# Kernel tuning notes

Hardware: AMD Instinct MI355X
Metric: run time of the kernel (lower is better)

Reference implementation:

```python
import jax, jax.numpy as jnp
import numpy as np

K = 8  # 2^3 kernel offsets for kernel-size-2, stride-2 transposed conv in 3D (HYPER_CUBE)
HID = 64


def sp_convT(x, W, parent, kofs):
    """Sparse generative transposed conv via kernel map.
    x: [Nin, Cin]; W: [K, Cin, Cout]; parent: [Nout] int; kofs: [Nout] int in [0,K).
    out[j] = x[parent[j]] @ W[kofs[j]].
    """
    xg = x[parent]  # [Nout, Cin] gather
    out = jnp.zeros((parent.shape[0], W.shape[2]), dtype=x.dtype)
    for k in range(K):  # fixed small structural loop over kernel offsets
        out = out + jnp.where((kofs == k)[:, None], xg @ W[k], jnp.zeros((), x.dtype))
    return out


def setup_inputs() -> dict:
    key = jax.random.key(0)
    ks = jax.random.split(key, 12)
    Ns = [5000, 20000, 80000, 320000]
    sc_i = 1.0 / np.sqrt(64)
    inp = {
        'x0': jax.random.normal(ks[0], (Ns[0], 64), jnp.float32),
        'x1': jax.random.normal(ks[1], (Ns[1], 64), jnp.float32),
        'x2': jax.random.normal(ks[2], (Ns[2], 64), jnp.float32),
        'W_i': jax.random.normal(ks[3], (K, 64, 4 * HID), jnp.float32) * sc_i,
        'W_h': jax.random.normal(ks[4], (K, HID, 4 * HID), jnp.float32) * sc_i,
        'W_c': jax.random.normal(ks[5], (K, HID, HID), jnp.float32) * sc_i,
        'parent0': jax.random.randint(ks[6], (Ns[1],), 0, Ns[0], jnp.int32),
        'kofs0': jax.random.randint(ks[7], (Ns[1],), 0, K, jnp.int32),
        'parent1': jax.random.randint(ks[8], (Ns[2],), 0, Ns[1], jnp.int32),
        'kofs1': jax.random.randint(ks[9], (Ns[2],), 0, K, jnp.int32),
        'parent2': jax.random.randint(ks[10], (Ns[3],), 0, Ns[2], jnp.int32),
        'kofs2': jax.random.randint(ks[11], (Ns[3],), 0, K, jnp.int32),
    }
    return inp


def reference(x0, x1, x2, W_i, W_h, W_c, parent0, kofs0, parent1, kofs1, parent2, kofs2):
    xs = [x0, x1, x2]
    parents = [parent0, parent1, parent2]
    kofss = [kofs0, kofs1, kofs2]
    hx = jnp.zeros((x0.shape[0], HID), dtype=x0.dtype)
    cx = jnp.zeros((x0.shape[0], HID), dtype=x0.dtype)
    for t in range(3):  # coder_num timesteps (structural loop)
        p, ko = parents[t], kofss[t]
        cx = sp_convT(cx, W_c, p, ko)                                   # upsample cell state
        gates = sp_convT(hx, W_h, p, ko) + sp_convT(xs[t], W_i, p, ko)  # [Nout, 4*HID]
        in_g, fg, cg, og = jnp.split(gates, 4, axis=1)
        in_g = jax.nn.sigmoid(in_g)
        fg = jax.nn.sigmoid(fg)
        cg = jax.nn.sigmoid(cg)  # NOTE: original uses sigmoid (not tanh) for cell_gate
        og = jax.nn.sigmoid(og)
        cx = fg * cx + in_g * cg
        hx = og * jnp.tanh(cx)
    return hx
```

## Files before the change

### kernel.cpp

```cpp
#include <hip/hip_runtime.h>


#define KNUM 8
#define TM 32
#define STEP_THREADS 256

typedef __attribute__((ext_vector_type(8))) _Float16 f16x8;
typedef __attribute__((ext_vector_type(4))) float f32x4;

__device__ __forceinline__ float fsig(float x) {
  return __builtin_amdgcn_rcpf(1.0f + __expf(-x));
}
__device__ __forceinline__ float ftanh_(float x) {
  float e = __expf(2.0f * x);
  return 1.0f - 2.0f * __builtin_amdgcn_rcpf(e + 1.0f);
}
__device__ __forceinline__ f16x8 to_h8(float4 a, float4 b) {
  f16x8 r;
  r[0] = (_Float16)a.x; r[1] = (_Float16)a.y; r[2] = (_Float16)a.z; r[3] = (_Float16)a.w;
  r[4] = (_Float16)b.x; r[5] = (_Float16)b.y; r[6] = (_Float16)b.z; r[7] = (_Float16)b.w;
  return r;
}

__global__ void prep_kernel(const float* __restrict__ Wi, const float* __restrict__ Wh,
                            const float* __restrict__ Wc,
                            const float* __restrict__ x0, const float* __restrict__ x1,
                            const float* __restrict__ x2, int ne0, int ne1, int ne2,
                            const int* __restrict__ k0, int n0,
                            const int* __restrict__ k1, int n1,
                            const int* __restrict__ k2, int n2,
                            _Float16* __restrict__ WgT, _Float16* __restrict__ WcT,
                            _Float16* __restrict__ x0f, _Float16* __restrict__ x1f,
                            _Float16* __restrict__ x2f, int* __restrict__ counts) {
  __shared__ int sh[3 * KNUM];
  if (threadIdx.x < 3 * KNUM) sh[threadIdx.x] = 0;
  __syncthreads();
  int tid = blockIdx.x * blockDim.x + threadIdx.x;
  int stride = gridDim.x * blockDim.x;
  for (int idx = tid; idx < KNUM * 256 * 128; idx += stride) {
    int k  = idx >> 15;
    int co = (idx >> 7) & 255;
    int ci = idx & 127;
    float v = (ci < 64) ? Wh[(k * 64 + ci) * 256 + co]
                        : Wi[(k * 64 + ci - 64) * 256 + co];
    WgT[idx] = (_Float16)v;
  }
  for (int idx = tid; idx < KNUM * 64 * 64; idx += stride) {
    int k  = idx >> 12;
    int co = (idx >> 6) & 63;
    int ci = idx & 63;
    WcT[idx] = (_Float16)Wc[(k * 64 + ci) * 64 + co];
  }
  for (int i = tid; i < (ne0 >> 3); i += stride) {
    float4 a = ((const float4*)x0)[2 * i], b = ((const float4*)x0)[2 * i + 1];
    ((f16x8*)x0f)[i] = to_h8(a, b);
  }
  for (int i = tid; i < (ne1 >> 3); i += stride) {
    float4 a = ((const float4*)x1)[2 * i], b = ((const float4*)x1)[2 * i + 1];
    ((f16x8*)x1f)[i] = to_h8(a, b);
  }
  for (int i = tid; i < (ne2 >> 3); i += stride) {
    float4 a = ((const float4*)x2)[2 * i], b = ((const float4*)x2)[2 * i + 1];
    ((f16x8*)x2f)[i] = to_h8(a, b);
  }
  for (int i = tid; i < n0; i += stride) atomicAdd(&sh[k0[i]], 1);
  for (int i = tid; i < n1; i += stride) atomicAdd(&sh[KNUM + k1[i]], 1);
  for (int i = tid; i < n2; i += stride) atomicAdd(&sh[2 * KNUM + k2[i]], 1);
  __syncthreads();
  if (threadIdx.x < 3 * KNUM && sh[threadIdx.x]) atomicAdd(&counts[threadIdx.x], sh[threadIdx.x]);
}

__device__ __forceinline__ void seg_select(int b, int& seg, int& rb, int& nb) {
  if (b < 32)       { seg = 0; rb = b;       nb = 32;  }
  else if (b < 160) { seg = 1; rb = b - 32;  nb = 128; }
  else              { seg = 2; rb = b - 160; nb = 352; }
}

__global__ void scatter_all_kernel(const int* __restrict__ k0, const int* __restrict__ p0, int n0,
                                   int2* __restrict__ op0,
                                   const int* __restrict__ k1, const int* __restrict__ p1, int n1,
                                   int2* __restrict__ op1,
                                   const int* __restrict__ k2, const int* __restrict__ p2, int n2,
                                   int2* __restrict__ op2,
                                   const int* __restrict__ counts, int* __restrict__ cursor) {
  int seg, rb, nb;
  seg_select(blockIdx.x, seg, rb, nb);
  const int* kp = seg == 0 ? k0 : seg == 1 ? k1 : k2;
  const int* pp = seg == 0 ? p0 : seg == 1 ? p1 : p2;
  int n = seg == 0 ? n0 : seg == 1 ? n1 : n2;
  int2* op = seg == 0 ? op0 : seg == 1 ? op1 : op2;

  __shared__ int h[KNUM], base[KNUM];
  if (threadIdx.x < KNUM) h[threadIdx.x] = 0;
  __syncthreads();
  int chunk = (n + nb - 1) / nb;
  int c0 = rb * chunk;
  int c1 = min(n, c0 + chunk);
  for (int i = c0 + threadIdx.x; i < c1; i += blockDim.x)
    atomicAdd(&h[kp[i]], 1);
  __syncthreads();
  if (threadIdx.x < KNUM) {
    int offk = 0;
    for (int k = 0; k < (int)threadIdx.x; ++k) offk += counts[seg * KNUM + k];
    base[threadIdx.x] = offk + atomicAdd(&cursor[seg * KNUM + threadIdx.x], h[threadIdx.x]);
    h[threadIdx.x] = 0;
  }
  __syncthreads();
  for (int i = c0 + threadIdx.x; i < c1; i += blockDim.x) {
    int k = kp[i];
    int pos = base[k] + atomicAdd(&h[k], 1);
    op[pos] = make_int2(i, pp[i]);
  }
}

template <bool FIRST, bool LAST>
__global__ __launch_bounds__(STEP_THREADS)
void lstm_step_kernel(const _Float16* __restrict__ xf, const _Float16* __restrict__ hc_in,
                      const int2* __restrict__ op, const int* __restrict__ counts,
                      const _Float16* __restrict__ WgT, const _Float16* __restrict__ WcT,
                      float* __restrict__ out32, _Float16* __restrict__ hc_out, int bpk) {
  __shared__ __align__(16) _Float16 A[TM][136];
  __shared__ __align__(16) _Float16 Cg[TM][72];
  __shared__ int jidx[TM];

  const int kb = blockIdx.x & 7;
  const int bi = blockIdx.x >> 3;
  int cnt = 0, off = 0;
#pragma unroll
  for (int k = 0; k < KNUM; ++k) {
    int c = counts[k];
    if (k < kb) off += c;
    if (k == kb) cnt = c;
  }
  const int ntiles = (cnt + TM - 1) / TM;
  if (bi >= ntiles) return;

  const int lane = threadIdx.x & 63;
  const int wcq  = threadIdx.x >> 6;
  const int l15  = lane & 15;
  const int kg   = lane >> 4;

  f16x8 bg[4][4];
  f16x8 bc[2];
  {
    const _Float16* wgp = WgT + (size_t)kb * (256 * 128);
#pragma unroll
    for (int g = 0; g < 4; ++g)
#pragma unroll
      for (int ks = (FIRST ? 2 : 0); ks < 4; ++ks)
        bg[g][ks] = *(const f16x8*)(wgp + (size_t)(64 * g + 16 * wcq + l15) * 128 + ks * 32 + kg * 8);
    if constexpr (!FIRST) {
      const _Float16* wcp = WcT + (size_t)kb * (64 * 64);
#pragma unroll
      for (int ks = 0; ks < 2; ++ks)
        bc[ks] = *(const f16x8*)(wcp + (size_t)(16 * wcq + l15) * 64 + ks * 32 + kg * 8);
    }
  }

  const int gr  = threadIdx.x >> 3;
  const int gq8 = threadIdx.x & 7;

  auto idx_of = [&](int tt) -> int2 {
    int grow = tt * TM + gr;
    bool v = (tt < ntiles) && (grow < cnt);
    int2 jp = op[off + min(grow, cnt - 1)];
    if (!v) jp.x = -1;
    return jp;
  };

  f16x8 xA{}, hA{}, cA{}; int jA = -1;
  f16x8 xB{}, hB{}, cB{}; int jB = -1;
  int2 jpP;

  auto rows_into = [&](int2 jp, f16x8& rx, f16x8& rh, f16x8& rc, int& rj) {
    int p = jp.y;
    rx = *(const f16x8*)(xf + (size_t)p * 64 + gq8 * 8);
    if constexpr (!FIRST) {
      const _Float16* hr = hc_in + (size_t)p * 128 + gq8 * 8;
      rh = *(const f16x8*)(hr);
      rc = *(const f16x8*)(hr + 64);
    }
    rj = jp.x;
  };

  rows_into(idx_of(bi), xA, hA, cA, jA);
  rows_into(idx_of(bi + bpk), xB, hB, cB, jB);
  jpP = idx_of(bi + 2 * bpk);

#define HALF_STEP(TCUR, RX, RH, RC, RJ)                                         \
  {                                                                             \
    asm volatile("s_barrier" ::: "memory");                                     \
    if (gq8 == 0) jidx[gr] = RJ;                                                \
    *(f16x8*)&A[gr][64 + gq8 * 8] = RX;                                         \
    if constexpr (!FIRST) {                                                     \
      *(f16x8*)&A[gr][gq8 * 8]  = RH;                                           \
      *(f16x8*)&Cg[gr][gq8 * 8] = RC;                                           \
    }                                                                           \
    asm volatile("s_waitcnt lgkmcnt(0)\n\ts_barrier" ::: "memory");             \
    rows_into(jpP, RX, RH, RC, RJ);            \
    jpP = idx_of((TCUR) + 3 * bpk);       \
    f32x4 aG[2][4];                                                             \
    f32x4 aC[2];                                                                \
    _Pragma("unroll")                                                           \
    for (int rf = 0; rf < 2; ++rf) {                                            \
      _Pragma("unroll")                                                         \
      for (int g = 0; g < 4; ++g) aG[rf][g] = f32x4{0.f, 0.f, 0.f, 0.f};        \
      aC[rf] = f32x4{0.f, 0.f, 0.f, 0.f};                                       \
    }                                                                           \
    _Pragma("unroll")                                                           \
    for (int ks = (FIRST ? 2 : 0); ks < 4; ++ks) {                              \
      _Pragma("unroll")                                                         \
      for (int rf = 0; rf < 2; ++rf) {                                          \
        f16x8 a = *(const f16x8*)&A[16 * rf + l15][ks * 32 + kg * 8];           \
        aG[rf][0] = __builtin_amdgcn_mfma_f32_16x16x32_f16(a, bg[0][ks], aG[rf][0], 0, 0, 0); \
        aG[rf][1] = __builtin_amdgcn_mfma_f32_16x16x32_f16(a, bg[1][ks], aG[rf][1], 0, 0, 0); \
        aG[rf][2] = __builtin_amdgcn_mfma_f32_16x16x32_f16(a, bg[2][ks], aG[rf][2], 0, 0, 0); \
        aG[rf][3] = __builtin_amdgcn_mfma_f32_16x16x32_f16(a, bg[3][ks], aG[rf][3], 0, 0, 0); \
      }                                                                         \
    }                                                                           \
    if constexpr (!FIRST) {                                                     \
      _Pragma("unroll")                                                         \
      for (int ks = 0; ks < 2; ++ks) {                                          \
        _Pragma("unroll")                                                       \
        for (int rf = 0; rf < 2; ++rf) {                                        \
          f16x8 a = *(const f16x8*)&Cg[16 * rf + l15][ks * 32 + kg * 8];        \
          aC[rf] = __builtin_amdgcn_mfma_f32_16x16x32_f16(a, bc[ks], aC[rf], 0, 0, 0); \
        }                                                                       \
      }                                                                         \
    }                                                                           \
    _Pragma("unroll")                                                           \
    for (int rf = 0; rf < 2; ++rf) {                                            \
      _Pragma("unroll")                                                         \
      for (int r = 0; r < 4; ++r) {                                             \
        int row = 16 * rf + kg * 4 + r;                                         \
        int j = jidx[row];                                                      \
        if (j < 0) continue;                                                    \
        float ing = fsig(aG[rf][0][r]);                                         \
        float fg  = fsig(aG[rf][1][r]);                                         \
        float cgt = fsig(aG[rf][2][r]);                                         \
        float og  = fsig(aG[rf][3][r]);                                         \
        float cup = FIRST ? 0.0f : aC[rf][r];                                   \
        float cxv = fg * cup + ing * cgt;                                       \
        float hxv = og * ftanh_(cxv);                                           \
        int ch = 16 * wcq + l15;                                                \
        if constexpr (LAST) {                                                   \
          out32[(size_t)j * 64 + ch] = hxv;                                     \
        } else {                                                                \
          hc_out[(size_t)j * 128 + ch]      = (_Float16)hxv;                    \
          hc_out[(size_t)j * 128 + 64 + ch] = (_Float16)cxv;                    \
        }                                                                       \
      }                                                                         \
    }                                                                           \
  }

  for (int t = bi; t < ntiles; t += 2 * bpk) {
    HALF_STEP(t, xA, hA, cA, jA);
    if (t + bpk < ntiles) {
      HALF_STEP(t + bpk, xB, hB, cB, jB);
    }
  }
#undef HALF_STEP
}

static inline int idiv_up(int a, int b) { return (a + b - 1) / b; }

template <bool FIRST, bool LAST>
static void run_step(const _Float16* xf, const _Float16* hc_in,
                     const int2* op, int nout, const int* counts,
                     const _Float16* WgT, const _Float16* WcT,
                     float* out32, _Float16* hc_out, hipStream_t stream) {
  int bpk = idiv_up(nout, KNUM * TM);
  if (bpk > 128) bpk = 128;
  if (bpk < 1) bpk = 1;
  lstm_step_kernel<FIRST, LAST><<<dim3(KNUM * bpk), dim3(STEP_THREADS), 0, stream>>>(
      xf, hc_in, op, counts, WgT, WcT, out32, hc_out, bpk);
}

extern "C" void kernel_launch(void* const* d_in, const int* in_sizes, int n_in,
                              void* d_out, int out_size, void* d_ws, size_t ws_size,
                              hipStream_t stream) {
  const float* x0 = (const float*)d_in[0];
  const float* x1 = (const float*)d_in[1];
  const float* x2 = (const float*)d_in[2];
  const float* Wi = (const float*)d_in[3];
  const float* Wh = (const float*)d_in[4];
  const float* Wc = (const float*)d_in[5];
  const int* parent0 = (const int*)d_in[6];
  const int* kofs0   = (const int*)d_in[7];
  const int* parent1 = (const int*)d_in[8];
  const int* kofs1   = (const int*)d_in[9];
  const int* parent2 = (const int*)d_in[10];
  const int* kofs2   = (const int*)d_in[11];
  const int N1 = in_sizes[6];
  const int N2 = in_sizes[8];
  const int N3 = in_sizes[10];
  const int ne0 = in_sizes[0], ne1 = in_sizes[1], ne2 = in_sizes[2];

  char* w = (char*)d_ws;
  auto carve = [&](size_t bytes) {
    char* p = w;
    w += (bytes + 255) & ~(size_t)255;
    return p;
  };
  _Float16* WgT = (_Float16*)carve((size_t)KNUM * 256 * 128 * 2);
  _Float16* WcT = (_Float16*)carve((size_t)KNUM * 64 * 64 * 2);
  int* ctrs     = (int*)carve(6 * KNUM * sizeof(int));
  int* counts   = ctrs;
  int* cursor   = ctrs + 3 * KNUM;
  _Float16* x0f = (_Float16*)carve((size_t)ne0 * 2);
  _Float16* x1f = (_Float16*)carve((size_t)ne1 * 2);
  _Float16* x2f = (_Float16*)carve((size_t)ne2 * 2);
  int2* op0     = (int2*)carve((size_t)N1 * sizeof(int2));
  int2* op1     = (int2*)carve((size_t)N2 * sizeof(int2));
  int2* op2     = (int2*)carve((size_t)N3 * sizeof(int2));
  _Float16* hc_a = (_Float16*)carve((size_t)N1 * 128 * 2);
  _Float16* hc_b = (_Float16*)carve((size_t)N2 * 128 * 2);
  (void)ws_size; (void)n_in; (void)out_size;

  hipMemsetAsync(ctrs, 0, 6 * KNUM * sizeof(int), stream);
  prep_kernel<<<1024, 256, 0, stream>>>(Wi, Wh, Wc, x0, x1, x2, ne0, ne1, ne2,
                                        kofs0, N1, kofs1, N2, kofs2, N3,
                                        WgT, WcT, x0f, x1f, x2f, counts);
  scatter_all_kernel<<<512, 256, 0, stream>>>(kofs0, parent0, N1, op0,
                                              kofs1, parent1, N2, op1,
                                              kofs2, parent2, N3, op2,
                                              counts, cursor);

  run_step<true, false>(x0f, nullptr, op0, N1, counts + 0 * KNUM,
                        WgT, WcT, nullptr, hc_a, stream);
  run_step<false, false>(x1f, hc_a, op1, N2, counts + 1 * KNUM,
                         WgT, WcT, nullptr, hc_b, stream);
  run_step<false, true>(x2f, hc_b, op2, N3, counts + 2 * KNUM,
                        WgT, WcT, (float*)d_out, nullptr, stream);
}
```

Baseline: 122.4 us.

## Load MFMA A-operands directly from global into registers, drop LDS staging

```diff
diff --git a/kernel.cpp b/kernel.cpp
--- a/kernel.cpp
+++ b/kernel.cpp
@@ -2,7 +2,7 @@
 
 
 #define KNUM 8
-#define TM 32
+#define TM 16
 #define STEP_THREADS 256
 
 typedef __attribute__((ext_vector_type(8))) _Float16 f16x8;
@@ -119,9 +119,7 @@
                       const int2* __restrict__ op, const int* __restrict__ counts,
                       const _Float16* __restrict__ WgT, const _Float16* __restrict__ WcT,
                       float* __restrict__ out32, _Float16* __restrict__ hc_out, int bpk) {
-  __shared__ __align__(16) _Float16 A[TM][136];
-  __shared__ __align__(16) _Float16 Cg[TM][72];
-  __shared__ int jidx[TM];
+  constexpr int NKS = FIRST ? 2 : 4;
 
   const int kb = blockIdx.x & 7;
   const int bi = blockIdx.x >> 3;
@@ -140,126 +138,138 @@
   const int l15  = lane & 15;
   const int kg   = lane >> 4;
 
-  f16x8 bg[4][4];
+  f16x8 bg[4][NKS];
   f16x8 bc[2];
   {
-    const _Float16* wgp = WgT + (size_t)kb * (256 * 128);
+    const _Float16* wgp = WgT + (size_t)kb * (256 * 128) + (FIRST ? 64 : 0) + kg * 8;
 #pragma unroll
     for (int g = 0; g < 4; ++g)
 #pragma unroll
-      for (int ks = (FIRST ? 2 : 0); ks < 4; ++ks)
-        bg[g][ks] = *(const f16x8*)(wgp + (size_t)(64 * g + 16 * wcq + l15) * 128 + ks * 32 + kg * 8);
+      for (int s = 0; s < NKS; ++s)
+        bg[g][s] = *(const f16x8*)(wgp + (size_t)(64 * g + 16 * wcq + l15) * 128 + s * 32);
     if constexpr (!FIRST) {
-      const _Float16* wcp = WcT + (size_t)kb * (64 * 64);
+      const _Float16* wcp = WcT + (size_t)kb * (64 * 64) + kg * 8;
 #pragma unroll
-      for (int ks = 0; ks < 2; ++ks)
-        bc[ks] = *(const f16x8*)(wcp + (size_t)(16 * wcq + l15) * 64 + ks * 32 + kg * 8);
+      for (int s = 0; s < 2; ++s)
+        bc[s] = *(const f16x8*)(wcp + (size_t)(16 * wcq + l15) * 64 + s * 32);
     }
   }
 
-  const int gr  = threadIdx.x >> 3;
-  const int gq8 = threadIdx.x & 7;
-
-  auto idx_of = [&](int tt) -> int2 {
-    int grow = tt * TM + gr;
-    bool v = (tt < ntiles) && (grow < cnt);
-    int2 jp = op[off + min(grow, cnt - 1)];
-    if (!v) jp.x = -1;
-    return jp;
+  auto ld_jp = [&](int tt) -> int2 {
+    return op[off + min(tt * TM + l15, cnt - 1)];
   };
 
-  f16x8 xA{}, hA{}, cA{}; int jA = -1;
-  f16x8 xB{}, hB{}, cB{}; int jB = -1;
-  int2 jpP;
-
-  auto rows_into = [&](int2 jp, f16x8& rx, f16x8& rh, f16x8& rc, int& rj) {
-    int p = jp.y;
-    rx = *(const f16x8*)(xf + (size_t)p * 64 + gq8 * 8);
-    if constexpr (!FIRST) {
-      const _Float16* hr = hc_in + (size_t)p * 128 + gq8 * 8;
-      rh = *(const f16x8*)(hr);
-      rc = *(const f16x8*)(hr + 64);
+  f16x8 Ax0{}, Ax1{}, Ah0{}, Ah1{}, Ac0{}, Ac1{};
+  int Aj0 = -1, Aj1 = -1, Aj2 = -1, Aj3 = -1;
+  f16x8 Bx0{}, Bx1{}, Bh0{}, Bh1{}, Bc0{}, Bc1{};
+  int Bj0 = -1, Bj1 = -1, Bj2 = -1, Bj3 = -1;
+  int2 iA, iB;
+
+#define ISSUE_SET(TT, S, JP)                                                   \
+  {                                                                            \
+    int p_ = (JP).y;                                                           \
+    const _Float16* xr_ = xf + (size_t)p_ * 64 + kg * 8;                       \
+    S##x0 = *(const f16x8*)(xr_);                                              \
+    S##x1 = *(const f16x8*)(xr_ + 32);                                         \
+    if constexpr (!FIRST) {                                                    \
+      const _Float16* hr_ = hc_in + (size_t)p_ * 128 + kg * 8;                 \
+      S##h0 = *(const f16x8*)(hr_);                                            \
+      S##h1 = *(const f16x8*)(hr_ + 32);                                       \
+      S##c0 = *(const f16x8*)(hr_ + 64);                                       \
+      S##c1 = *(const f16x8*)(hr_ + 96);                                       \
+    }                                                                          \
+    int base_ = (TT) * TM + kg * 4;                                            \
+    if ((TT) * TM + TM <= cnt) {                                               \
+      S##j0 = op[off + base_ + 0].x;                                           \
+      S##j1 = op[off + base_ + 1].x;                                           \
+      S##j2 = op[off + base_ + 2].x;                                           \
+      S##j3 = op[off + base_ + 3].x;                                           \
+    } else {                                                                   \
+      S##j0 = (base_ + 0 < cnt) ? op[off + base_ + 0].x : -1;                  \
+      S##j1 = (base_ + 1 < cnt) ? op[off + base_ + 1].x : -1;                  \
+      S##j2 = (base_ + 2 < cnt) ? op[off + base_ + 2].x : -1;                  \
+      S##j3 = (base_ + 3 < cnt) ? op[off + base_ + 3].x : -1;                  \
+    }                                                                          \
+  }
+
+#define TILE_STEP(TT, S, IS)                                                   \
+  {                                                                            \
+    f32x4 aG0{0.f, 0.f, 0.f, 0.f}, aG1{0.f, 0.f, 0.f, 0.f};                    \
+    f32x4 aG2{0.f, 0.f, 0.f, 0.f}, aG3{0.f, 0.f, 0.f, 0.f};                    \
+    f32x4 aC{0.f, 0.f, 0.f, 0.f};                                              \
+    __builtin_amdgcn_s_setprio(1);                                             \
+    if constexpr (FIRST) {                                                     \
+      aG0 = __builtin_amdgcn_mfma_f32_16x16x32_f16(S##x0, bg[0][0], aG0, 0, 0, 0); \
+      aG1 = __builtin_amdgcn_mfma_f32_16x16x32_f16(S##x0, bg[1][0], aG1, 0, 0, 0); \
+      aG2 = __builtin_amdgcn_mfma_f32_16x16x32_f16(S##x0, bg[2][0], aG2, 0, 0, 0); \
+      aG3 = __builtin_amdgcn_mfma_f32_16x16x32_f16(S##x0, bg[3][0], aG3, 0, 0, 0); \
+      aG0 = __builtin_amdgcn_mfma_f32_16x16x32_f16(S##x1, bg[0][1], aG0, 0, 0, 0); \
+      aG1 = __builtin_amdgcn_mfma_f32_16x16x32_f16(S##x1, bg[1][1], aG1, 0, 0, 0); \
+      aG2 = __builtin_amdgcn_mfma_f32_16x16x32_f16(S##x1, bg[2][1], aG2, 0, 0, 0); \
+      aG3 = __builtin_amdgcn_mfma_f32_16x16x32_f16(S##x1, bg[3][1], aG3, 0, 0, 0); \
+    } else {                                                                   \
+      aG0 = __builtin_amdgcn_mfma_f32_16x16x32_f16(S##h0, bg[0][0], aG0, 0, 0, 0); \
+      aG1 = __builtin_amdgcn_mfma_f32_16x16x32_f16(S##h0, bg[1][0], aG1, 0, 0, 0); \
+      aG2 = __builtin_amdgcn_mfma_f32_16x16x32_f16(S##h0, bg[2][0], aG2, 0, 0, 0); \
+      aG3 = __builtin_amdgcn_mfma_f32_16x16x32_f16(S##h0, bg[3][0], aG3, 0, 0, 0); \
+      aG0 = __builtin_amdgcn_mfma_f32_16x16x32_f16(S##h1, bg[0][1], aG0, 0, 0, 0); \
+      aG1 = __builtin_amdgcn_mfma_f32_16x16x32_f16(S##h1, bg[1][1], aG1, 0, 0, 0); \
+      aG2 = __builtin_amdgcn_mfma_f32_16x16x32_f16(S##h1, bg[2][1], aG2, 0, 0, 0); \
+      aG3 = __builtin_amdgcn_mfma_f32_16x16x32_f16(S##h1, bg[3][1], aG3, 0, 0, 0); \
+      aG0 = __builtin_amdgcn_mfma_f32_16x16x32_f16(S##x0, bg[0][2], aG0, 0, 0, 0); \
+      aG1 = __builtin_amdgcn_mfma_f32_16x16x32_f16(S##x0, bg[1][2], aG1, 0, 0, 0); \
+      aG2 = __builtin_amdgcn_mfma_f32_16x16x32_f16(S##x0, bg[2][2], aG2, 0, 0, 0); \
+      aG3 = __builtin_amdgcn_mfma_f32_16x16x32_f16(S##x0, bg[3][2], aG3, 0, 0, 0); \
+      aG0 = __builtin_amdgcn_mfma_f32_16x16x32_f16(S##x1, bg[0][3], aG0, 0, 0, 0); \
+      aG1 = __builtin_amdgcn_mfma_f32_16x16x32_f16(S##x1, bg[1][3], aG1, 0, 0, 0); \
+      aG2 = __builtin_amdgcn_mfma_f32_16x16x32_f16(S##x1, bg[2][3], aG2, 0, 0, 0); \
+      aG3 = __builtin_amdgcn_mfma_f32_16x16x32_f16(S##x1, bg[3][3], aG3, 0, 0, 0); \
+      aC  = __builtin_amdgcn_mfma_f32_16x16x32_f16(S##c0, bc[0], aC, 0, 0, 0); \
+      aC  = __builtin_amdgcn_mfma_f32_16x16x32_f16(S##c1, bc[1], aC, 0, 0, 0); \
+    }                                                                          \
+    __builtin_amdgcn_s_setprio(0);                                             \
+    int tj0 = S##j0, tj1 = S##j1, tj2 = S##j2, tj3 = S##j3;                    \
+    ISSUE_SET((TT) + 2 * bpk, S, IS);                                          \
+    IS = ld_jp((TT) + 4 * bpk);                                                \
+    __builtin_amdgcn_sched_barrier(0);                                         \
+    _Pragma("unroll")                                                          \
+    for (int r = 0; r < 4; ++r) {                                              \
+      int j = (r == 0) ? tj0 : (r == 1) ? tj1 : (r == 2) ? tj2 : tj3;          \
+      if (j < 0) continue;                                                     \
+      float ing = fsig(aG0[r]);                                                \
+      float fg  = fsig(aG1[r]);                                                \
+      float cgt = fsig(aG2[r]);              \
+      float og  = fsig(aG3[r]);                                                \
+      float cup = FIRST ? 0.0f : aC[r];                                        \
+      float cxv = fg * cup + ing * cgt;                                        \
+      float hxv = og * ftanh_(cxv);                                            \
+      int ch = 16 * wcq + l15;                                                 \
+      if constexpr (LAST) {                                                    \
+        out32[(size_t)j * 64 + ch] = hxv;                                      \
+      } else {                                                                 \
+        hc_out[(size_t)j * 128 + ch]      = (_Float16)hxv;                     \
+        hc_out[(size_t)j * 128 + 64 + ch] = (_Float16)cxv;                     \
+      }                                                                        \
+    }                                                                          \
+  }
+
+  {
+    int2 jp0 = ld_jp(bi);
+    ISSUE_SET(bi, A, jp0);
+    int2 jp1 = ld_jp(bi + bpk);
+    ISSUE_SET(bi + bpk, B, jp1);
+    iA = ld_jp(bi + 2 * bpk);
+    iB = ld_jp(bi + 3 * bpk);
+  }
+
+  for (int t = bi; t < ntiles; t += 2 * bpk) {
+    TILE_STEP(t, A, iA);
+    if (t + bpk < ntiles) {
+      TILE_STEP(t + bpk, B, iB);
     }
-    rj = jp.x;
-  };
-
-  rows_into(idx_of(bi), xA, hA, cA, jA);
-  rows_into(idx_of(bi + bpk), xB, hB, cB, jB);
-  jpP = idx_of(bi + 2 * bpk);
-
-#define HALF_STEP(TCUR, RX, RH, RC, RJ)                                         \
-  {                                                                             \
-    asm volatile("s_barrier" ::: "memory");                                     \
-    if (gq8 == 0) jidx[gr] = RJ;                                                \
-    *(f16x8*)&A[gr][64 + gq8 * 8] = RX;                                         \
-    if constexpr (!FIRST) {                                                     \
-      *(f16x8*)&A[gr][gq8 * 8]  = RH;                                           \
-      *(f16x8*)&Cg[gr][gq8 * 8] = RC;                                           \
-    }                                                                           \
-    asm volatile("s_waitcnt lgkmcnt(0)\n\ts_barrier" ::: "memory");             \
-    rows_into(jpP, RX, RH, RC, RJ);            \
-    jpP = idx_of((TCUR) + 3 * bpk);       \
-    f32x4 aG[2][4];                                                             \
-    f32x4 aC[2];                                                                \
-    _Pragma("unroll")                                                           \
-    for (int rf = 0; rf < 2; ++rf) {                                            \
-      _Pragma("unroll")                                                         \
-      for (int g = 0; g < 4; ++g) aG[rf][g] = f32x4{0.f, 0.f, 0.f, 0.f};        \
-      aC[rf] = f32x4{0.f, 0.f, 0.f, 0.f};                                       \
-    }                                                                           \
-    _Pragma("unroll")                                                           \
-    for (int ks = (FIRST ? 2 : 0); ks < 4; ++ks) {                              \
-      _Pragma("unroll")                                                         \
-      for (int rf = 0; rf < 2; ++rf) {                                          \
-        f16x8 a = *(const f16x8*)&A[16 * rf + l15][ks * 32 + kg * 8];           \
-        aG[rf][0] = __builtin_amdgcn_mfma_f32_16x16x32_f16(a, bg[0][ks], aG[rf][0], 0, 0, 0); \
-        aG[rf][1] = __builtin_amdgcn_mfma_f32_16x16x32_f16(a, bg[1][ks], aG[rf][1], 0, 0, 0); \
-        aG[rf][2] = __builtin_amdgcn_mfma_f32_16x16x32_f16(a, bg[2][ks], aG[rf][2], 0, 0, 0); \
-        aG[rf][3] = __builtin_amdgcn_mfma_f32_16x16x32_f16(a, bg[3][ks], aG[rf][3], 0, 0, 0); \
-      }                                                                         \
-    }                                                                           \
-    if constexpr (!FIRST) {                                                     \
-      _Pragma("unroll")                                                         \
-      for (int ks = 0; ks < 2; ++ks) {                                          \
-        _Pragma("unroll")                                                       \
-        for (int rf = 0; rf < 2; ++rf) {                                        \
-          f16x8 a = *(const f16x8*)&Cg[16 * rf + l15][ks * 32 + kg * 8];        \
-          aC[rf] = __builtin_amdgcn_mfma_f32_16x16x32_f16(a, bc[ks], aC[rf], 0, 0, 0); \
-        }                                                                       \
-      }                                                                         \
-    }                                                                           \
-    _Pragma("unroll")                                                           \
-    for (int rf = 0; rf < 2; ++rf) {                                            \
-      _Pragma("unroll")                                                         \
-      for (int r = 0; r < 4; ++r) {                                             \
-        int row = 16 * rf + kg * 4 + r;                                         \
-        int j = jidx[row];                                                      \
-        if (j < 0) continue;                                                    \
-        float ing = fsig(aG[rf][0][r]);                                         \
-        float fg  = fsig(aG[rf][1][r]);                                         \
-        float cgt = fsig(aG[rf][2][r]);                                         \
-        float og  = fsig(aG[rf][3][r]);                                         \
-        float cup = FIRST ? 0.0f : aC[rf][r];                                   \
-        float cxv = fg * cup + ing * cgt;                                       \
-        float hxv = og * ftanh_(cxv);                                           \
-        int ch = 16 * wcq + l15;                                                \
-        if constexpr (LAST) {                                                   \
-          out32[(size_t)j * 64 + ch] = hxv;                                     \
-        } else {                                                                \
-          hc_out[(size_t)j * 128 + ch]      = (_Float16)hxv;                    \
-          hc_out[(size_t)j * 128 + 64 + ch] = (_Float16)cxv;                    \
-        }                                                                       \
-      }                                                                         \
-    }                                                                           \
-  }
-
-  for (int t = bi; t < ntiles; t += 2 * bpk) {
-    HALF_STEP(t, xA, hA, cA, jA);
-    if (t + bpk < ntiles) {
-      HALF_STEP(t + bpk, xB, hB, cB, jB);
-    }
-  }
-#undef HALF_STEP
+  }
+#undef TILE_STEP
+#undef ISSUE_SET
 }
 
 static inline int idiv_up(int a, int b) { return (a + b - 1) / b; }
```

New measurement: 162.6 us. 1.33x slower.

## Interleave x with h/c rows and stage outputs in LDS for coalesced stores

Applied to the files above, without the earlier changes.

```diff
diff --git a/kernel.cpp b/kernel.cpp
--- a/kernel.cpp
+++ b/kernel.cpp
@@ -30,8 +30,8 @@
                             const int* __restrict__ k1, int n1,
                             const int* __restrict__ k2, int n2,
                             _Float16* __restrict__ WgT, _Float16* __restrict__ WcT,
-                            _Float16* __restrict__ x0f, _Float16* __restrict__ x1f,
-                            _Float16* __restrict__ x2f, int* __restrict__ counts) {
+                            _Float16* __restrict__ x0f, _Float16* __restrict__ xhcA,
+                            _Float16* __restrict__ xhcB, int* __restrict__ counts) {
   __shared__ int sh[3 * KNUM];
   if (threadIdx.x < 3 * KNUM) sh[threadIdx.x] = 0;
   __syncthreads();
@@ -57,11 +57,13 @@
   }
   for (int i = tid; i < (ne1 >> 3); i += stride) {
     float4 a = ((const float4*)x1)[2 * i], b = ((const float4*)x1)[2 * i + 1];
-    ((f16x8*)x1f)[i] = to_h8(a, b);
+    int row = i >> 3, c = i & 7;
+    *(f16x8*)(xhcA + (size_t)row * 192 + 128 + c * 8) = to_h8(a, b);
   }
   for (int i = tid; i < (ne2 >> 3); i += stride) {
     float4 a = ((const float4*)x2)[2 * i], b = ((const float4*)x2)[2 * i + 1];
-    ((f16x8*)x2f)[i] = to_h8(a, b);
+    int row = i >> 3, c = i & 7;
+    *(f16x8*)(xhcB + (size_t)row * 192 + 128 + c * 8) = to_h8(a, b);
   }
   for (int i = tid; i < n0; i += stride) atomicAdd(&sh[k0[i]], 1);
   for (int i = tid; i < n1; i += stride) atomicAdd(&sh[KNUM + k1[i]], 1);
@@ -115,13 +117,17 @@
 
 template <bool FIRST, bool LAST>
 __global__ __launch_bounds__(STEP_THREADS)
-void lstm_step_kernel(const _Float16* __restrict__ xf, const _Float16* __restrict__ hc_in,
+void lstm_step_kernel(const _Float16* __restrict__ xin,
                       const int2* __restrict__ op, const int* __restrict__ counts,
                       const _Float16* __restrict__ WgT, const _Float16* __restrict__ WcT,
-                      float* __restrict__ out32, _Float16* __restrict__ hc_out, int bpk) {
+                      float* __restrict__ out32, _Float16* __restrict__ xhc_out, int bpk) {
   __shared__ __align__(16) _Float16 A[TM][136];
   __shared__ __align__(16) _Float16 Cg[TM][72];
   __shared__ int jidx[TM];
+  __shared__ __align__(16) char Obuf[9216];
+  float (*O32)[68] = (float(*)[68])Obuf;
+  _Float16 (*Oh)[72] = (_Float16(*)[72])Obuf;
+  _Float16 (*Oc)[72] = (_Float16(*)[72])(Obuf + 32 * 72 * 2);
 
   const int kb = blockIdx.x & 7;
   const int bi = blockIdx.x >> 3;
@@ -135,8 +141,9 @@
   const int ntiles = (cnt + TM - 1) / TM;
   if (bi >= ntiles) return;
 
-  const int lane = threadIdx.x & 63;
-  const int wcq  = threadIdx.x >> 6;
+  const int tid  = threadIdx.x;
+  const int lane = tid & 63;
+  const int wcq  = tid >> 6;
   const int l15  = lane & 15;
   const int kg   = lane >> 4;
 
@@ -157,10 +164,10 @@
     }
   }
 
-  const int gr  = threadIdx.x >> 3;
-  const int gq8 = threadIdx.x & 7;
-
-  auto idx_of = [&](int tt) -> int2 {
+  const int gr  = tid >> 3;
+  const int gq8 = tid & 7;
+
+  auto ld_jp = [&](int tt) -> int2 {
     int grow = tt * TM + gr;
     bool v = (tt < ntiles) && (grow < cnt);
     int2 jp = op[off + min(grow, cnt - 1)];
@@ -174,22 +181,24 @@
 
   auto rows_into = [&](int2 jp, f16x8& rx, f16x8& rh, f16x8& rc, int& rj) {
     int p = jp.y;
-    rx = *(const f16x8*)(xf + (size_t)p * 64 + gq8 * 8);
-    if constexpr (!FIRST) {
-      const _Float16* hr = hc_in + (size_t)p * 128 + gq8 * 8;
-      rh = *(const f16x8*)(hr);
-      rc = *(const f16x8*)(hr + 64);
+    if constexpr (FIRST) {
+      rx = *(const f16x8*)(xin + (size_t)p * 64 + gq8 * 8);
+    } else {
+      const _Float16* r_ = xin + (size_t)p * 192 + gq8 * 8;
+      rh = *(const f16x8*)(r_);
+      rc = *(const f16x8*)(r_ + 64);
+      rx = *(const f16x8*)(r_ + 128);
     }
     rj = jp.x;
   };
 
-  rows_into(idx_of(bi), xA, hA, cA, jA);
-  rows_into(idx_of(bi + bpk), xB, hB, cB, jB);
-  jpP = idx_of(bi + 2 * bpk);
+  rows_into(ld_jp(bi), xA, hA, cA, jA);
+  rows_into(ld_jp(bi + bpk), xB, hB, cB, jB);
+  jpP = ld_jp(bi + 2 * bpk);
 
 #define HALF_STEP(TCUR, RX, RH, RC, RJ)                                         \
   {                                                                             \
-    asm volatile("s_barrier" ::: "memory");                                     \
+    asm volatile("s_barrier" ::: "memory");         \
     if (gq8 == 0) jidx[gr] = RJ;                                                \
     *(f16x8*)&A[gr][64 + gq8 * 8] = RX;                                         \
     if constexpr (!FIRST) {                                                     \
@@ -197,8 +206,8 @@
       *(f16x8*)&Cg[gr][gq8 * 8] = RC;                                           \
     }                                                                           \
     asm volatile("s_waitcnt lgkmcnt(0)\n\ts_barrier" ::: "memory");             \
-    rows_into(jpP, RX, RH, RC, RJ);            \
-    jpP = idx_of((TCUR) + 3 * bpk);       \
+    rows_into(jpP, RX, RH, RC, RJ);               \
+    jpP = ld_jp((TCUR) + 3 * bpk);                                              \
     f32x4 aG[2][4];                                                             \
     f32x4 aC[2];                                                                \
     _Pragma("unroll")                                                           \
@@ -228,26 +237,46 @@
         }                                                                       \
       }                                                                         \
     }                                                                           \
+                              \
     _Pragma("unroll")                                                           \
     for (int rf = 0; rf < 2; ++rf) {                                            \
       _Pragma("unroll")                                                         \
       for (int r = 0; r < 4; ++r) {                                             \
-        int row = 16 * rf + kg * 4 + r;                                         \
-        int j = jidx[row];                                                      \
-        if (j < 0) continue;                                                    \
+        int row = 16 * rf + kg * 4 + r;           \
         float ing = fsig(aG[rf][0][r]);                                         \
         float fg  = fsig(aG[rf][1][r]);                                         \
-        float cgt = fsig(aG[rf][2][r]);                                         \
+        float cgt = fsig(aG[rf][2][r]);       \
         float og  = fsig(aG[rf][3][r]);                                         \
         float cup = FIRST ? 0.0f : aC[rf][r];                                   \
         float cxv = fg * cup + ing * cgt;                                       \
         float hxv = og * ftanh_(cxv);                                           \
         int ch = 16 * wcq + l15;                                                \
         if constexpr (LAST) {                                                   \
-          out32[(size_t)j * 64 + ch] = hxv;                                     \
+          O32[row][ch] = hxv;                                                   \
         } else {                                                                \
-          hc_out[(size_t)j * 128 + ch]      = (_Float16)hxv;                    \
-          hc_out[(size_t)j * 128 + 64 + ch] = (_Float16)cxv;                    \
+          Oh[row][ch] = (_Float16)hxv;                                          \
+          Oc[row][ch] = (_Float16)cxv;                                          \
+        }                                                                       \
+      }                                                                         \
+    }                                                                           \
+    asm volatile("s_waitcnt lgkmcnt(0)\n\ts_barrier" ::: "memory");             \
+           \
+    {                                                                           \
+      int srow = tid >> 3, sc = tid & 7;                                        \
+      int j = jidx[srow];                                                       \
+      if (j >= 0) {                                                             \
+        if constexpr (LAST) {                                                   \
+          f32x4 v0 = *(const f32x4*)&O32[srow][sc * 8];                         \
+          f32x4 v1 = *(const f32x4*)&O32[srow][sc * 8 + 4];                     \
+          float* dst = out32 + (size_t)j * 64 + sc * 8;                         \
+          *(f32x4*)dst = v0;                                                    \
+          *(f32x4*)(dst + 4) = v1;                                              \
+        } else {                                                                \
+          f16x8 vh = *(const f16x8*)&Oh[srow][sc * 8];                          \
+          f16x8 vc = *(const f16x8*)&Oc[srow][sc * 8];                          \
+          _Float16* dst = xhc_out + (size_t)j * 192 + sc * 8;                   \
+          *(f16x8*)dst = vh;                                                    \
+          *(f16x8*)(dst + 64) = vc;                                             \
         }                                                                       \
       }                                                                         \
     }                                                                           \
@@ -265,15 +294,14 @@
 static inline int idiv_up(int a, int b) { return (a + b - 1) / b; }
 
 template <bool FIRST, bool LAST>
-static void run_step(const _Float16* xf, const _Float16* hc_in,
-                     const int2* op, int nout, const int* counts,
+static void run_step(const _Float16* xin, const int2* op, int nout, const int* counts,
                      const _Float16* WgT, const _Float16* WcT,
-                     float* out32, _Float16* hc_out, hipStream_t stream) {
+                     float* out32, _Float16* xhc_out, hipStream_t stream) {
   int bpk = idiv_up(nout, KNUM * TM);
-  if (bpk > 128) bpk = 128;
+  if (bpk > 160) bpk = 160;
   if (bpk < 1) bpk = 1;
   lstm_step_kernel<FIRST, LAST><<<dim3(KNUM * bpk), dim3(STEP_THREADS), 0, stream>>>(
-      xf, hc_in, op, counts, WgT, WcT, out32, hc_out, bpk);
+      xin, op, counts, WgT, WcT, out32, xhc_out, bpk);
 }
 
 extern "C" void kernel_launch(void* const* d_in, const int* in_sizes, int n_in,
@@ -308,28 +336,26 @@
   int* counts   = ctrs;
   int* cursor   = ctrs + 3 * KNUM;
   _Float16* x0f = (_Float16*)carve((size_t)ne0 * 2);
-  _Float16* x1f = (_Float16*)carve((size_t)ne1 * 2);
-  _Float16* x2f = (_Float16*)carve((size_t)ne2 * 2);
   int2* op0     = (int2*)carve((size_t)N1 * sizeof(int2));
   int2* op1     = (int2*)carve((size_t)N2 * sizeof(int2));
   int2* op2     = (int2*)carve((size_t)N3 * sizeof(int2));
-  _Float16* hc_a = (_Float16*)carve((size_t)N1 * 128 * 2);
-  _Float16* hc_b = (_Float16*)carve((size_t)N2 * 128 * 2);
+  _Float16* xhc_a = (_Float16*)carve((size_t)N1 * 192 * 2);
+  _Float16* xhc_b = (_Float16*)carve((size_t)N2 * 192 * 2);
   (void)ws_size; (void)n_in; (void)out_size;
 
   hipMemsetAsync(ctrs, 0, 6 * KNUM * sizeof(int), stream);
   prep_kernel<<<1024, 256, 0, stream>>>(Wi, Wh, Wc, x0, x1, x2, ne0, ne1, ne2,
                                         kofs0, N1, kofs1, N2, kofs2, N3,
-                                        WgT, WcT, x0f, x1f, x2f, counts);
+                                        WgT, WcT, x0f, xhc_a, xhc_b, counts);
   scatter_all_kernel<<<512, 256, 0, stream>>>(kofs0, parent0, N1, op0,
                                               kofs1, parent1, N2, op1,
                                               kofs2, parent2, N3, op2,
                                               counts, cursor);
 
-  run_step<true, false>(x0f, nullptr, op0, N1, counts + 0 * KNUM,
-                        WgT, WcT, nullptr, hc_a, stream);
-  run_step<false, false>(x1f, hc_a, op1, N2, counts + 1 * KNUM,
-                         WgT, WcT, nullptr, hc_b, stream);
-  run_step<false, true>(x2f, hc_b, op2, N3, counts + 2 * KNUM,
+  run_step<true, false>(x0f, op0, N1, counts + 0 * KNUM,
+                        WgT, WcT, nullptr, xhc_a, stream);
+  run_step<false, false>(xhc_a, op1, N2, counts + 1 * KNUM,
+                         WgT, WcT, nullptr, xhc_b, stream);
+  run_step<false, true>(xhc_b, op2, N3, counts + 2 * KNUM,
                         WgT, WcT, (float*)d_out, nullptr, stream);
 }
```

New measurement: 116.9 us. 4.5% less time.
